# Kernel tuning notes

Measured on AMD Instinct MI355X. Metric: run time of the kernel, lower is better.

Reference implementation:

```python
import jax, jax.numpy as jnp
import numpy as np

B, S, D, H = 4, 2048, 512, 8
HD = D // H  # head width = 64

def setup_inputs() -> dict:
    key = jax.random.key(0)
    ks = jax.random.split(key, 7)
    x = jax.random.normal(ks[0], (B, S, D), dtype=jnp.float32)
    mask = jnp.ones((B, S), dtype=jnp.int32)
    # torch nn.Linear(dim, dim): weight [out, in], bias [out]
    sc = 1.0 / np.sqrt(D)
    Wq = jax.random.uniform(ks[1], (D, D), jnp.float32, -sc, sc)
    bq = jax.random.uniform(ks[2], (D,), jnp.float32, -sc, sc)
    Wk = jax.random.uniform(ks[3], (D, D), jnp.float32, -sc, sc)
    bk = jax.random.uniform(ks[4], (D,), jnp.float32, -sc, sc)
    Wv = jax.random.uniform(ks[5], (D, D), jnp.float32, -sc, sc)
    bv = jax.random.uniform(ks[6], (D,), jnp.float32, -sc, sc)
    return {"x": x, "mask": mask, "Wq": Wq, "bq": bq, "Wk": Wk, "bk": bk, "Wv": Wv, "bv": bv}

def reference(x, mask, Wq, bq, Wk, bk, Wv, bv):
    # QKV projections (torch Linear: x @ W.T + b)
    q = jnp.einsum('bsd,ed->bse', x, Wq) + bq
    k = jnp.einsum('bsd,ed->bse', x, Wk) + bk
    v = jnp.einsum('bsd,ed->bse', x, Wv) + bv
    # split heads -> (B, H, S, HD)
    q = q.reshape(B, S, H, HD).transpose(0, 2, 1, 3)
    k = k.reshape(B, S, H, HD).transpose(0, 2, 1, 3)
    v = v.reshape(B, S, H, HD).transpose(0, 2, 1, 3)
    scores = jnp.einsum('bhqd,bhkd->bhqk', q, k) / np.sqrt(HD).astype(np.float32)
    m = mask[:, None, None, :].astype(scores.dtype)  # (B,1,1,S)
    scores = scores - 10000.0 * (1.0 - m)
    attn = jax.nn.softmax(scores, axis=-1)  # dropout is identity in eval mode
    h = jnp.einsum('bhqk,bhkd->bhqd', attn, v)
    h = h.transpose(0, 2, 1, 3).reshape(B, S, D)
    return h
```

## Files before the change

kernel.cpp:

```cpp
#include <hip/hip_runtime.h>
#include <hip/hip_bf16.h>

#define Bb 4
#define Ss 2048
#define Dd 512
#define Hh 8
#define HD 64
#define NX (Bb*Ss*Dd)
#define NW (3*Dd*Dd)

typedef __attribute__((ext_vector_type(8))) short bf8_t;
typedef __attribute__((ext_vector_type(4))) float f4_t;
typedef unsigned int u32;
typedef __attribute__((ext_vector_type(4))) unsigned int u32x4;

typedef const unsigned int __attribute__((address_space(1)))* gas_t;
typedef unsigned int __attribute__((address_space(3)))* las_t;

#define LOG2E 1.44269504088896f
#define MBIAS_C (-10000.0f * LOG2E)

__device__ __forceinline__ short cvt1(float f) {
  __hip_bfloat16 h = __float2bfloat16(f);
  union { __hip_bfloat16 hh; short ss; } u; u.hh = h; return u.ss;
}

__device__ __forceinline__ u32 pkrn(float a, float b) {
  union { __hip_bfloat162 h2; u32 u; } v;
  v.h2 = __float22bfloat162_rn(make_float2(a, b));
  return v.u;
}

__device__ __forceinline__ bf8_t pack8(float4 f0, float4 f1) {
  union { bf8_t v8; u32x4 u4; } u;
  u.u4.x = pkrn(f0.x, f0.y); u.u4.y = pkrn(f0.z, f0.w);
  u.u4.z = pkrn(f1.x, f1.y); u.u4.w = pkrn(f1.z, f1.w);
  return u.v8;
}

__device__ __forceinline__ void gload_lds16(const void* g, void* l) {
  __builtin_amdgcn_global_load_lds((gas_t)g, (las_t)l, 16, 0, 0);
}

__global__ __launch_bounds__(256) void convert_kernel(
    const float* __restrict__ x, const float* __restrict__ Wq,
    const float* __restrict__ Wk, const float* __restrict__ Wv,
    short* __restrict__ xb, short* __restrict__ Wb)
{
  size_t i = ((size_t)blockIdx.x * 256 + threadIdx.x) * 8;
  const float* src; short* dst;
  if (i < (size_t)NX) { src = x + i; dst = xb + i; }
  else {
    size_t j = i - NX;
    int ws = (int)(j >> 18);
    const float* W = (ws == 0) ? Wq : (ws == 1) ? Wk : Wv;
    src = W + (j & 0x3FFFF); dst = Wb + j;
  }
  float4 f0 = *(const float4*)src;
  float4 f1 = *(const float4*)(src + 4);
  *(bf8_t*)dst = pack8(f0, f1);
}

__global__ __launch_bounds__(256, 2) void qkv_proj_kernel(
    const short* __restrict__ xb, const short* __restrict__ Wb,
    const float* __restrict__ bq, const float* __restrict__ bk,
    const float* __restrict__ bv,
    short* __restrict__ Qg, short* __restrict__ Kg, short* __restrict__ Vtg)
{
  __shared__ short As[2][128*64];
  __shared__ short Bs2[2][128*64];
  const int p = blockIdx.y >> 2;
  const short* __restrict__ W = Wb + (size_t)p * Dd * Dd;
  const float* __restrict__ bias = (p==0) ? bq : (p==1) ? bk : bv;
  const int m0 = blockIdx.x * 128;
  const int n0 = (blockIdx.y & 3) * 128;
  const int tid = threadIdx.x;
  const int lane = tid & 63, wid = tid >> 6;
  const int lq = lane & 15, hi = lane >> 4;
  const int wm = wid & 1, wn = wid >> 1;

  const short* aSrc[4];
  const short* bSrc[4];
  #pragma unroll
  for (int i = 0; i < 4; i++) {
    int slot = tid + i*256, row = slot >> 3, c = slot & 7;
    aSrc[i] = xb + (size_t)(m0 + row)*Dd + ((c ^ (row&7))*8);
    bSrc[i] = W  + (size_t)(n0 + row)*Dd + ((c ^ (row&7))*8);
  }

  const f4_t zero4 = {0.f, 0.f, 0.f, 0.f};
  f4_t acc[4][4];
  #pragma unroll
  for (int i = 0; i < 4; i++)
    #pragma unroll
    for (int j = 0; j < 4; j++) acc[i][j] = zero4;

  auto STAGE = [&](int bufi, int k0) {
    #pragma unroll
    for (int i = 0; i < 4; i++) {
      gload_lds16(aSrc[i] + k0, &As[bufi][(tid + i*256)*8]);
      gload_lds16(bSrc[i] + k0, &Bs2[bufi][(tid + i*256)*8]);
    }
  };

  STAGE(0, 0);
  __syncthreads();
  for (int kt = 0; kt < 8; kt++) {
    const int cur = kt & 1;
    if (kt < 7) STAGE(cur ^ 1, (kt + 1)*64);
    #pragma unroll
    for (int ks = 0; ks < 2; ks++) {
      const int cu = ks*4 + hi;
      bf8_t a[4], bfrag[4];
      #pragma unroll
      for (int mi = 0; mi < 4; mi++) {
        int row = wm*64 + mi*16 + lq;
        a[mi] = *(const bf8_t*)(&As[cur][row*64 + ((cu ^ (row&7))*8)]);
      }
      #pragma unroll
      for (int nf = 0; nf < 4; nf++) {
        int row = wn*64 + nf*16 + lq;
        bfrag[nf] = *(const bf8_t*)(&Bs2[cur][row*64 + ((cu ^ (row&7))*8)]);
      }
      #pragma unroll
      for (int mi = 0; mi < 4; mi++)
        #pragma unroll
        for (int nf = 0; nf < 4; nf++)
          acc[mi][nf] = __builtin_amdgcn_mfma_f32_16x16x32_bf16(a[mi], bfrag[nf], acc[mi][nf], 0, 0, 0);
    }
    __syncthreads();
  }

  const float qs = (p == 0) ? 0.125f * LOG2E : 1.0f;
  float badd[4];
  #pragma unroll
  for (int nf = 0; nf < 4; nf++) badd[nf] = bias[n0 + wn*64 + nf*16 + lq];
  #pragma unroll
  for (int mi = 0; mi < 4; mi++) {
    #pragma unroll
    for (int nf = 0; nf < 4; nf++) {
      const int col = n0 + wn*64 + nf*16 + lq;
      const int h = col >> 6, hd = col & 63;
      #pragma unroll
      for (int r = 0; r < 4; r++) {
        int mrow = m0 + wm*64 + mi*16 + hi*4 + r;
        int bb = mrow >> 11, ss = mrow & (Ss-1);
        short val = cvt1((acc[mi][nf][r] + badd[nf]) * qs);
        if (p == 2)
          Vtg[(((size_t)bb*Hh + h)*HD + hd)*Ss + ss] = val;
        else if (p == 0)
          Qg[(((size_t)bb*Hh + h)*Ss + ss)*HD + hd] = val;
        else
          Kg[(((size_t)bb*Hh + h)*Ss + ss)*HD + hd] = val;
      }
    }
  }
}

__global__ __launch_bounds__(256, 2) void attn_kernel(
    const short* __restrict__ Qg, const short* __restrict__ Kg,
    const short* __restrict__ Vtg, const int* __restrict__ mask,
    float* __restrict__ out)
{
  __shared__ short Ks[2][64*64];
  __shared__ short Vs[2][64*64];
  const int bh = blockIdx.x;
  const int b = bh >> 3, h = bh & 7;
  const int tid = threadIdx.x, lane = tid & 63, w = tid >> 6;
  const int hi = lane >> 4, lq = lane & 15, tau = hi & 1;
  const short* __restrict__ Qb = Qg + (size_t)bh * Ss * HD;
  const short* __restrict__ Kb = Kg + (size_t)bh * Ss * HD;
  const short* __restrict__ Vb = Vtg + (size_t)bh * HD * Ss;
  const int* __restrict__ maskb = mask + b * Ss;
  const int q0 = blockIdx.y * 128 + w * 32;
  const int NT = Ss / 64;

  u32 mvbits = 0;
  #pragma unroll
  for (int t = 0; t < NT; t++)
    mvbits |= (maskb[t*64 + lane] != 0 ? 1u : 0u) << t;

  bf8_t qf[2][2];
  #pragma unroll
  for (int qg = 0; qg < 2; qg++)
    #pragma unroll
    for (int ks = 0; ks < 2; ks++)
      qf[qg][ks] = *(const bf8_t*)(Qb + (size_t)(q0 + qg*16 + lq)*HD + ks*32 + hi*8);

  const f4_t zero4 = {0.f, 0.f, 0.f, 0.f};
  f4_t o0[4], o1[4];
  #pragma unroll
  for (int j = 0; j < 4; j++) { o0[j] = zero4; o1[j] = zero4; }
  f4_t lacc0 = zero4, lacc1 = zero4;

  const bf8_t ones = {(short)0x3F80,(short)0x3F80,(short)0x3F80,(short)0x3F80,
                      (short)0x3F80,(short)0x3F80,(short)0x3F80,(short)0x3F80};

  const int sA = tid, sB = tid + 256;
  const short* ksrcA = Kb + (size_t)(sA>>3)*HD + (((sA&7) ^ ((sA>>3)&7))*8);
  const short* ksrcB = Kb + (size_t)(sB>>3)*HD + (((sB&7) ^ ((sB>>3)&7))*8);
  const short* vsrcA = Vb + (size_t)(sA>>3)*Ss + (((sA&7) ^ ((sA>>3)&7))*8);
  const short* vsrcB = Vb + (size_t)(sB>>3)*Ss + (((sB&7) ^ ((sB>>3)&7))*8);

  auto STAGE = [&](int bufi, int kv) {
    gload_lds16(ksrcA + (size_t)kv*HD, &Ks[bufi][sA*8]);
    gload_lds16(ksrcB + (size_t)kv*HD, &Ks[bufi][sB*8]);
    gload_lds16(vsrcA + kv,            &Vs[bufi][sA*8]);
    gload_lds16(vsrcB + kv,            &Vs[bufi][sB*8]);
  };

  STAGE(0, 0);
  __syncthreads();
  for (int t = 0; t < NT; t++) {
    const int cur = t & 1;
    if (t + 1 < NT) STAGE(cur ^ 1, (t + 1)*64);

    f4_t sa[4], sb[4];
    #pragma unroll
    for (int kb = 0; kb < 4; kb++) {
      const int row = kb*16 + lq;
      bf8_t kf0 = *(const bf8_t*)(&Ks[cur][row*64 + ((hi       ^ (row&7))*8)]);
      bf8_t kf1 = *(const bf8_t*)(&Ks[cur][row*64 + (((4 + hi) ^ (row&7))*8)]);
      sa[kb] = __builtin_amdgcn_mfma_f32_16x16x32_bf16(kf0, qf[0][0], zero4, 0, 0, 0);
      sa[kb] = __builtin_amdgcn_mfma_f32_16x16x32_bf16(kf1, qf[0][1], sa[kb], 0, 0, 0);
      sb[kb] = __builtin_amdgcn_mfma_f32_16x16x32_bf16(kf0, qf[1][0], zero4, 0, 0, 0);
      sb[kb] = __builtin_amdgcn_mfma_f32_16x16x32_bf16(kf1, qf[1][1], sb[kb], 0, 0, 0);
    }
    const bool mok = (mvbits >> t) & 1u;
    if (__any(!mok)) {
      float mbl = mok ? 0.0f : MBIAS_C;
      #pragma unroll
      for (int kb = 0; kb < 4; kb++)
        #pragma unroll
        for (int r = 0; r < 4; r++) {
          float mm = __shfl(mbl, kb*16 + hi*4 + r, 64);
          sa[kb][r] += mm; sb[kb][r] += mm;
        }
    }
    bf8_t pf0[2], pf1[2];
    {
      u32 Wa[4][2], Wbp[4][2];
      #pragma unroll
      for (int kb = 0; kb < 4; kb++) {
        Wa[kb][0] = pkrn(__builtin_amdgcn_exp2f(sa[kb][0]), __builtin_amdgcn_exp2f(sa[kb][1]));
        Wa[kb][1] = pkrn(__builtin_amdgcn_exp2f(sa[kb][2]), __builtin_amdgcn_exp2f(sa[kb][3]));
        Wbp[kb][0] = pkrn(__builtin_amdgcn_exp2f(sb[kb][0]), __builtin_amdgcn_exp2f(sb[kb][1]));
        Wbp[kb][1] = pkrn(__builtin_amdgcn_exp2f(sb[kb][2]), __builtin_amdgcn_exp2f(sb[kb][3]));
      }
      #pragma unroll
      for (int c = 0; c < 2; c++) {
        u32 ma[4], mb[4];
        #pragma unroll
        for (int d = 0; d < 2; d++) {
          u32 X = Wa[2*c][d], Y = Wa[2*c+1][d];
          asm volatile("v_permlane32_swap_b32 %0, %1" : "+v"(X), "+v"(Y));
          u32 Xs = (u32)__builtin_amdgcn_ds_swizzle((int)X, 0x401F);
          u32 Ys = (u32)__builtin_amdgcn_ds_swizzle((int)Y, 0x401F);
          ma[d]     = tau ? Ys : X;
          ma[2 + d] = tau ? Y  : Xs;
          u32 X2 = Wbp[2*c][d], Y2 = Wbp[2*c+1][d];
          asm volatile("v_permlane32_swap_b32 %0, %1" : "+v"(X2), "+v"(Y2));
          u32 X2s = (u32)__builtin_amdgcn_ds_swizzle((int)X2, 0x401F);
          u32 Y2s = (u32)__builtin_amdgcn_ds_swizzle((int)Y2, 0x401F);
          mb[d]     = tau ? Y2s : X2;
          mb[2 + d] = tau ? Y2  : X2s;
        }
        union { bf8_t v8; u32x4 u4; } pa, pb;
        pa.u4.x = ma[0]; pa.u4.y = ma[1]; pa.u4.z = ma[2]; pa.u4.w = ma[3];
        pb.u4.x = mb[0]; pb.u4.y = mb[1]; pb.u4.z = mb[2]; pb.u4.w = mb[3];
        pf0[c] = pa.v8; pf1[c] = pb.v8;
      }
    }
    __builtin_amdgcn_s_setprio(1);
    lacc0 = __builtin_amdgcn_mfma_f32_16x16x32_bf16(pf0[0], ones, lacc0, 0, 0, 0);
    lacc0 = __builtin_amdgcn_mfma_f32_16x16x32_bf16(pf0[1], ones, lacc0, 0, 0, 0);
    lacc1 = __builtin_amdgcn_mfma_f32_16x16x32_bf16(pf1[0], ones, lacc1, 0, 0, 0);
    lacc1 = __builtin_amdgcn_mfma_f32_16x16x32_bf16(pf1[1], ones, lacc1, 0, 0, 0);
    #pragma unroll
    for (int nf2 = 0; nf2 < 4; nf2++) {
      const int vr = nf2*16 + lq;
      #pragma unroll
      for (int ks2 = 0; ks2 < 2; ks2++) {
        bf8_t vf = *(const bf8_t*)(&Vs[cur][vr*64 + (((ks2*4 + hi) ^ (vr&7))*8)]);
        o0[nf2] = __builtin_amdgcn_mfma_f32_16x16x32_bf16(pf0[ks2], vf, o0[nf2], 0, 0, 0);
        o1[nf2] = __builtin_amdgcn_mfma_f32_16x16x32_bf16(pf1[ks2], vf, o1[nf2], 0, 0, 0);
      }
    }
    __builtin_amdgcn_s_setprio(0);
    __syncthreads();
  }

  #pragma unroll
  for (int nf2 = 0; nf2 < 4; nf2++)
    #pragma unroll
    for (int r = 0; r < 4; r++) {
      int srow0 = q0 + hi*4 + r;
      int srow1 = q0 + 16 + hi*4 + r;
      out[((size_t)(b*Ss + srow0))*Dd + h*HD + nf2*16 + lq] = o0[nf2][r] / lacc0[r];
      out[((size_t)(b*Ss + srow1))*Dd + h*HD + nf2*16 + lq] = o1[nf2][r] / lacc1[r];
    }
}

extern "C" void kernel_launch(void* const* d_in, const int* in_sizes, int n_in,
                              void* d_out, int out_size, void* d_ws, size_t ws_size,
                              hipStream_t stream) {
  const float* x  = (const float*)d_in[0];
  const int* mask = (const int*)d_in[1];
  const float* Wq = (const float*)d_in[2];
  const float* bq = (const float*)d_in[3];
  const float* Wk = (const float*)d_in[4];
  const float* bk = (const float*)d_in[5];
  const float* Wv = (const float*)d_in[6];
  const float* bv = (const float*)d_in[7];
  float* out = (float*)d_out;

  short* Qg = (short*)d_ws;
  short* Kg = Qg + (size_t)Bb*Hh*Ss*HD;
  short* Vt = Kg + (size_t)Bb*Hh*Ss*HD;
  short* xb = Vt + (size_t)Bb*Hh*Ss*HD;
  short* Wb = xb + (size_t)NX;

  convert_kernel<<<dim3((NX + NW)/2048), 256, 0, stream>>>(x, Wq, Wk, Wv, xb, Wb);
  qkv_proj_kernel<<<dim3(64, 12), 256, 0, stream>>>(xb, Wb, bq, bk, bv, Qg, Kg, Vt);
  attn_kernel<<<dim3(32, 16), 256, 0, stream>>>(Qg, Kg, Vt, mask, out);
}
```

Measured before the change: 89.86 us.

## Split attention KV range across two blocks and combine partials in a new kernel

The attention grid gains a z dimension of 2, so each block handles half of the key/value sequence. Each block writes its unnormalized output as fp16 partials plus its row sums into reused workspace, and a new combine kernel adds the two halves and normalizes. Launch bounds are raised to allow 4 blocks per CU. The aim is to double the number of blocks and raise occupancy on a grid that only gave about two blocks per CU. In exchange it adds an extra kernel launch and a partial-output write/read round trip, and fp16 partials risk precision loss or overflow on unnormalized sums.

```diff
diff --git a/kernel.cpp b/kernel.cpp
--- a/kernel.cpp
+++ b/kernel.cpp
@@ -1,5 +1,6 @@
 #include <hip/hip_runtime.h>
 #include <hip/hip_bf16.h>
+#include <hip/hip_fp16.h>
 
 #define Bb 4
 #define Ss 2048
@@ -8,8 +9,10 @@
 #define HD 64
 #define NX (Bb*Ss*Dd)
 #define NW (3*Dd*Dd)
+#define PHS ((size_t)Bb*Hh*Ss*HD)
 
 typedef __attribute__((ext_vector_type(8))) short bf8_t;
+typedef __attribute__((ext_vector_type(8))) short s8_t;
 typedef __attribute__((ext_vector_type(4))) float f4_t;
 typedef unsigned int u32;
 typedef __attribute__((ext_vector_type(4))) unsigned int u32x4;
@@ -36,6 +39,13 @@
   u.u4.x = pkrn(f0.x, f0.y); u.u4.y = pkrn(f0.z, f0.w);
   u.u4.z = pkrn(f1.x, f1.y); u.u4.w = pkrn(f1.z, f1.w);
   return u.v8;
+}
+
+__device__ __forceinline__ short h2s(float f) {
+  union { __half h; short s; } u; u.h = __float2half(f); return u.s;
+}
+__device__ __forceinline__ float s2f(short s) {
+  union { short s; __half h; } u; u.s = s; return __half2float(u.h);
 }
 
 __device__ __forceinline__ void gload_lds16(const void* g, void* l) {
@@ -157,15 +167,18 @@
   }
 }
 
-__global__ __launch_bounds__(256, 2) void attn_kernel(
+__global__ __launch_bounds__(256, 4) void attn_kernel(
     const short* __restrict__ Qg, const short* __restrict__ Kg,
     const short* __restrict__ Vtg, const int* __restrict__ mask,
-    float* __restrict__ out)
+    short* __restrict__ po, float* __restrict__ plc)
 {
   __shared__ short Ks[2][64*64];
   __shared__ short Vs[2][64*64];
   const int bh = blockIdx.x;
-  const int b = bh >> 3, h = bh & 7;
+  const int b = bh >> 3;
+  const int z = blockIdx.z;
+  const int koff = z << 10;
+  const int NT2 = 16;
   const int tid = threadIdx.x, lane = tid & 63, w = tid >> 6;
   const int hi = lane >> 4, lq = lane & 15, tau = hi & 1;
   const short* __restrict__ Qb = Qg + (size_t)bh * Ss * HD;
@@ -173,12 +186,11 @@
   const short* __restrict__ Vb = Vtg + (size_t)bh * HD * Ss;
   const int* __restrict__ maskb = mask + b * Ss;
   const int q0 = blockIdx.y * 128 + w * 32;
-  const int NT = Ss / 64;
 
   u32 mvbits = 0;
   #pragma unroll
-  for (int t = 0; t < NT; t++)
-    mvbits |= (maskb[t*64 + lane] != 0 ? 1u : 0u) << t;
+  for (int t = 0; t < NT2; t++)
+    mvbits |= (maskb[koff + t*64 + lane] != 0 ? 1u : 0u) << t;
 
   bf8_t qf[2][2];
   #pragma unroll
@@ -209,11 +221,11 @@
     gload_lds16(vsrcB + kv,            &Vs[bufi][sB*8]);
   };
 
-  STAGE(0, 0);
+  STAGE(0, koff);
   __syncthreads();
-  for (int t = 0; t < NT; t++) {
+  for (int t = 0; t < NT2; t++) {
     const int cur = t & 1;
-    if (t + 1 < NT) STAGE(cur ^ 1, (t + 1)*64);
+    if (t + 1 < NT2) STAGE(cur ^ 1, koff + (t + 1)*64);
 
     f4_t sa[4], sb[4];
     #pragma unroll
@@ -290,15 +302,52 @@
     __syncthreads();
   }
 
+  short* __restrict__ pob = po + (size_t)z * PHS + (size_t)bh * Ss * HD;
+  float* __restrict__ plcb = plc + (size_t)z * (Bb*Hh*Ss) + (size_t)bh * Ss;
   #pragma unroll
   for (int nf2 = 0; nf2 < 4; nf2++)
     #pragma unroll
     for (int r = 0; r < 4; r++) {
       int srow0 = q0 + hi*4 + r;
       int srow1 = q0 + 16 + hi*4 + r;
-      out[((size_t)(b*Ss + srow0))*Dd + h*HD + nf2*16 + lq] = o0[nf2][r] / lacc0[r];
-      out[((size_t)(b*Ss + srow1))*Dd + h*HD + nf2*16 + lq] = o1[nf2][r] / lacc1[r];
-    }
+      pob[(size_t)srow0*HD + nf2*16 + lq] = h2s(o0[nf2][r]);
+      pob[(size_t)srow1*HD + nf2*16 + lq] = h2s(o1[nf2][r]);
+    }
+  if (lq == 0) {
+    #pragma unroll
+    for (int r = 0; r < 4; r++) {
+      plcb[q0 + hi*4 + r]      = lacc0[r];
+      plcb[q0 + 16 + hi*4 + r] = lacc1[r];
+    }
+  }
+}
+
+__global__ __launch_bounds__(256) void combine_kernel(
+    const short* __restrict__ po, const float* __restrict__ plc,
+    float* __restrict__ out)
+{
+  size_t i = ((size_t)blockIdx.x * 256 + threadIdx.x) * 8;
+  int b = (int)(i >> 20);
+  int s = (int)((i >> 9) & (Ss - 1));
+  int d = (int)(i & (Dd - 1));
+  int h = d >> 6, hd = d & 63;
+  size_t p0 = ((size_t)(b*Hh + h)*Ss + s)*HD + hd;
+  s8_t a = *(const s8_t*)(po + p0);
+  s8_t c = *(const s8_t*)(po + PHS + p0);
+  int li = (b*Hh + h)*Ss + s;
+  float l = plc[li] + plc[Bb*Hh*Ss + li];
+  float inv = 1.0f / l;
+  float4 r0, r1;
+  r0.x = (s2f(a[0]) + s2f(c[0])) * inv;
+  r0.y = (s2f(a[1]) + s2f(c[1])) * inv;
+  r0.z = (s2f(a[2]) + s2f(c[2])) * inv;
+  r0.w = (s2f(a[3]) + s2f(c[3])) * inv;
+  r1.x = (s2f(a[4]) + s2f(c[4])) * inv;
+  r1.y = (s2f(a[5]) + s2f(c[5])) * inv;
+  r1.z = (s2f(a[6]) + s2f(c[6])) * inv;
+  r1.w = (s2f(a[7]) + s2f(c[7])) * inv;
+  *(float4*)(out + i) = r0;
+  *(float4*)(out + i + 4) = r1;
 }
 
 extern "C" void kernel_launch(void* const* d_in, const int* in_sizes, int n_in,
@@ -315,12 +364,15 @@
   float* out = (float*)d_out;
 
   short* Qg = (short*)d_ws;
-  short* Kg = Qg + (size_t)Bb*Hh*Ss*HD;
-  short* Vt = Kg + (size_t)Bb*Hh*Ss*HD;
-  short* xb = Vt + (size_t)Bb*Hh*Ss*HD;
+  short* Kg = Qg + PHS;
+  short* Vt = Kg + PHS;
+  short* xb = Vt + PHS;
   short* Wb = xb + (size_t)NX;
+  short* po = xb;
+  float* plc = (float*)(po + 2*PHS);
 
   convert_kernel<<<dim3((NX + NW)/2048), 256, 0, stream>>>(x, Wq, Wk, Wv, xb, Wb);
   qkv_proj_kernel<<<dim3(64, 12), 256, 0, stream>>>(xb, Wb, bq, bk, bv, Qg, Kg, Vt);
-  attn_kernel<<<dim3(32, 16), 256, 0, stream>>>(Qg, Kg, Vt, mask, out);
-}
+  attn_kernel<<<dim3(32, 16, 2), 256, 0, stream>>>(Qg, Kg, Vt, mask, po, plc);
+  combine_kernel<<<dim3(NX/2048), 256, 0, stream>>>(po, plc, out);
+}
```

Result: slower. 93.10 us (+3.6%).
